# Optimization experiments

Measured on AMD Instinct MI355X. Metric: run time of the kernel, lower is better.

The kernel has to match this reference:

```python
import jax, jax.numpy as jnp
import numpy as np

B, A, HR = 2, 180, 512
H_OUT = W_OUT = 512


def setup_inputs() -> dict:
    key = jax.random.key(0)
    k1, = jax.random.split(key, 1)
    sino = jax.random.normal(k1, (B, A, HR), dtype=jnp.float32)
    angles_deg = jnp.linspace(0.0, 180.0, A, endpoint=False, dtype=jnp.float32)
    return {"sino": sino, "angles_deg": angles_deg, "H": H_OUT, "W": W_OUT}


def _forward(sino, angles_deg, H, W):
    Bn, An, Hr = sino.shape
    pad = int(1.0 * 0.1 * min(H, W))  # pad_ratio = 1.0
    Hp, Wp = H + 2 * pad, W + 2 * pad

    # --- F.interpolate bilinear, align_corners=False: (A,B,Hr,1) -> (A,B,Hp,Wp).
    # Input width is 1, so width interp replicates the single column; only height interp matters.
    src = jnp.clip((jnp.arange(Hp, dtype=jnp.float32) + 0.5) * (Hr / Hp) - 0.5, 0.0, Hr - 1)
    i0 = jnp.floor(src).astype(jnp.int32)
    i1 = jnp.minimum(i0 + 1, Hr - 1)
    wH = src - i0.astype(jnp.float32)
    p = jnp.transpose(sino, (1, 0, 2)).astype(jnp.float32)  # (A,B,Hr)
    col = p[:, :, i0] * (1.0 - wH) + p[:, :, i1] * wH       # (A,B,Hp)
    proj = jnp.broadcast_to(col[:, :, :, None], (An, Bn, Hp, Wp))  # (A,B,Hp,Wp)

    # --- affine_grid (align_corners=False), sign = -1
    th = -jnp.deg2rad(angles_deg)
    c, s = jnp.cos(th), jnp.sin(th)                          # (A,)
    xs = (jnp.arange(Wp, dtype=jnp.float32) + 0.5) * (2.0 / Wp) - 1.0
    ys = (jnp.arange(Hp, dtype=jnp.float32) + 0.5) * (2.0 / Hp) - 1.0
    gx = c[:, None, None] * xs[None, None, :] - s[:, None, None] * ys[None, :, None]  # (A,Hp,Wp)
    gy = s[:, None, None] * xs[None, None, :] + c[:, None, None] * ys[None, :, None]

    # --- grid_sample bilinear, zeros padding, align_corners=False
    ix = ((gx + 1.0) * Wp - 1.0) * 0.5
    iy = ((gy + 1.0) * Hp - 1.0) * 0.5
    x0 = jnp.floor(ix).astype(jnp.int32); x1 = x0 + 1
    y0 = jnp.floor(iy).astype(jnp.int32); y1 = y0 + 1
    wx = ix - x0.astype(jnp.float32)
    wy = iy - y0.astype(jnp.float32)

    def corner(img, xi, yi, w):  # img (B,Hp,Wp); idx/w (Hp,Wp)
        valid = (xi >= 0) & (xi <= Wp - 1) & (yi >= 0) & (yi <= Hp - 1)
        xc = jnp.clip(xi, 0, Wp - 1)
        yc = jnp.clip(yi, 0, Hp - 1)
        return img[:, yc, xc] * (w * valid.astype(jnp.float32))[None]

    def sample(img, x0a, x1a, y0a, y1a, wxa, wya):
        return (corner(img, x0a, y0a, (1 - wxa) * (1 - wya)) +
                corner(img, x1a, y0a, wxa * (1 - wya)) +
                corner(img, x0a, y1a, (1 - wxa) * wya) +
                corner(img, x1a, y1a, wxa * wya))

    xr = jax.vmap(sample)(proj, x0, x1, y0, y1, wx, wy)      # (A,B,Hp,Wp)
    acc = xr.sum(axis=0) / (An + 1e-06)                      # (B,Hp,Wp)
    acc = acc[:, None, :, :]                                 # (B,1,Hp,Wp)
    if pad > 0:
        acc = acc[:, :, pad:Hp - pad, pad:Wp - pad]
    return acc


def reference(sino, angles_deg, H, W):
    return _forward(sino, angles_deg, H, W)
```

## Files before the change

### kernel.cpp

```cpp
#include <hip/hip_runtime.h>
#include <hip/hip_fp16.h>
#include <math.h>

#define B_N   2
#define A_N   180
#define HR_N  512
#define H_OUT 512
#define W_OUT 512
#define PAD   51
#define HP    614
#define WP    614
#define GUARD 80
#define HPP   (HP + 2*GUARD)
#define NPIX  (H_OUT * W_OUT)

#define TILE  16
#define CH    30
#define NCH   (A_N / CH)
#define WIN   24


__device__ __forceinline__ float col_val(const float* __restrict__ sino,
                                         int b, int a, int yy) {
    if (yy < 0 || yy >= HP) return 0.0f;
    float src = ((float)yy + 0.5f) * ((float)HR_N / (float)HP) - 0.5f;
    src = fminf(fmaxf(src, 0.0f), (float)(HR_N - 1));
    int i0 = (int)floorf(src);
    int i1 = min(i0 + 1, HR_N - 1);
    float wH = src - (float)i0;
    const float* srow = sino + ((size_t)b * A_N + a) * HR_N;
    return srow[i0] * (1.0f - wH) + srow[i1] * wH;
}

__global__ void prep_kernel(const float* __restrict__ sino,
                            const float* __restrict__ angles,
                            uint2* __restrict__ pk2,
                            float2* __restrict__ tg) {
    int idx = blockIdx.x * blockDim.x + threadIdx.x;
    if (idx < A_N) {
        float th = -angles[idx] * (float)(M_PI / 180.0);
        tg[idx] = make_float2(cosf(th), sinf(th));
    }
    const int total = A_N * HPP;
    if (idx < total) {
        int y = idx % HPP;
        int a = idx / HPP;
        int yy = y - GUARD;
        float v00 = col_val(sino, 0, a, yy);
        float v10 = col_val(sino, 1, a, yy);
        float v01 = col_val(sino, 0, a, yy + 1);
        float v11 = col_val(sino, 1, a, yy + 1);
        __half2 lo = __floats2half2_rn(v00, v10);
        __half2 hi = __floats2half2_rn(v01, v11);
        uint2 u;
        u.x = *(unsigned int*)&lo;
        u.y = *(unsigned int*)&hi;
        pk2[idx] = u;
    }
}

template <bool INTERIOR>
__device__ __forceinline__ void bp_body(const uint2* __restrict__ pk2,
                                        const float2* __restrict__ tgv,
                                        uint2* __restrict__ s_win,
                                        const int* __restrict__ s_base,
                                        int t, float X, float Y, float Xc, float Yc,
                                        float& acc0, float& acc1) {
    for (int ch = 0; ch < NCH; ++ch) {
        int a0 = ch * CH;
        for (int e = t; e < CH * WIN; e += 256) {
            int la = e / WIN;
            int j  = e - la * WIN;
            int a  = a0 + la;
            s_win[e] = pk2[(size_t)a * HPP + (GUARD + s_base[a] + j)];
        }
        __syncthreads();

#pragma unroll 6
        for (int la = 0; la < CH; ++la) {
            float2 cs = tgv[a0 + la];
            float c = cs.x, s = cs.y;
            float iyc   = fmaf(s, Xc, fmaf(c, Yc, 306.5f));
            float basef = floorf(iyc);
            float iyp   = fmaf(s, X, fmaf(c, Y, 317.5f));
            float f  = iyp - basef;
            int   li = (int)f;
            float wy = f - (float)li;

            uint2 cv = s_win[la * WIN + li];
            __half2 lo = *(__half2*)&cv.x;
            __half2 hi = *(__half2*)&cv.y;
            float c00 = __low2float(lo), c10 = __high2float(lo);
            float c01 = __low2float(hi), c11 = __high2float(hi);

            if (INTERIOR) {
                acc0 = fmaf(wy, c01 - c00, acc0 + c00);
                acc1 = fmaf(wy, c11 - c10, acc1 + c10);
            } else {
                float ix = fmaf(c, X, fmaf(-s, Y, 306.5f));
                float xf = fminf(fmaxf(ix + 1.0f, 0.0f), 1.0f)
                         * fminf(fmaxf((float)WP - ix, 0.0f), 1.0f);
                float t0 = fmaf(wy, c01 - c00, c00);
                float t1 = fmaf(wy, c11 - c10, c10);
                acc0 = fmaf(xf, t0, acc0);
                acc1 = fmaf(xf, t1, acc1);
            }
        }
        __syncthreads();
    }
}

__global__ __launch_bounds__(256) void bp_kernel(const uint2* __restrict__ pk2,
                                                 const float2* __restrict__ tgv,
                                                 float* __restrict__ out) {
    __shared__ uint2 s_win[CH * WIN];
    __shared__ int   s_base[A_N];

    int t  = threadIdx.x;
    int tx = blockIdx.x, ty = blockIdx.y;
    float Xc = (float)(tx * TILE) - 248.0f;
    float Yc = (float)(ty * TILE) - 248.0f;

    if (t < A_N) {
        float2 cs = tgv[t];
        float iyc = fmaf(cs.y, Xc, fmaf(cs.x, Yc, 306.5f));
        s_base[t] = (int)floorf(iyc) - 11;
    }

    int lx = t & (TILE - 1);
    int ly = t >> 4;
    float X = (float)(tx * TILE + lx) - 255.5f;
    float Y = (float)(ty * TILE + ly) - 255.5f;

    float acc0 = 0.0f, acc1 = 0.0f;
    __syncthreads();

    bool interior = (Xc * Xc + Yc * Yc) <= 87500.0f;
    if (interior)
        bp_body<true >(pk2, tgv, s_win, s_base, t, X, Y, Xc, Yc, acc0, acc1);
    else
        bp_body<false>(pk2, tgv, s_win, s_base, t, X, Y, Xc, Yc, acc0, acc1);

    const float inv = 1.0f / (180.0f + 1e-6f);
    int idx = (ty * TILE + ly) * W_OUT + (tx * TILE + lx);
    out[idx]        = acc0 * inv;
    out[NPIX + idx] = acc1 * inv;
}

extern "C" void kernel_launch(void* const* d_in, const int* in_sizes, int n_in,
                              void* d_out, int out_size, void* d_ws, size_t ws_size,
                              hipStream_t stream) {
    const float* sino   = (const float*)d_in[0];
    const float* angles = (const float*)d_in[1];
    char*   ws  = (char*)d_ws;
    uint2*  pk2 = (uint2*)ws;
    float2* tg  = (float2*)(ws + (size_t)A_N * HPP * sizeof(uint2));

    const int total = A_N * HPP;
    prep_kernel<<<(total + 255) / 256, 256, 0, stream>>>(sino, angles, pk2, tg);

    dim3 grid(W_OUT / TILE, H_OUT / TILE);
    bp_kernel<<<grid, 256, 0, stream>>>(pk2, tg, (float*)d_out);
}
```

Measured before the change: 91.38 us.

## Split angle loop across two block halves with atomic accumulation

Each tile is now processed by two blocks, each handling half of the angles, and the partial sums are combined with atomicAdd into a zeroed output. This doubles the block count from 1024 to 2048 so more work is in flight per CU. It also precomputes per-angle cos, sin and window base in shared memory as a float4, removing per-iteration floor and recomputation. The cost is an extra memset, atomic writes, and duplicated per-block setup.

```diff
diff --git a/kernel.cpp b/kernel.cpp
--- a/kernel.cpp
+++ b/kernel.cpp
@@ -14,10 +14,11 @@
 #define HPP   (HP + 2*GUARD)
 #define NPIX  (H_OUT * W_OUT)
 
-#define TILE  16
-#define CH    30
-#define NCH   (A_N / CH)
-#define WIN   24
+#define TILE   16
+#define HALF_A 90
+#define CH     30
+#define NCHH   (HALF_A / CH)
+#define WIN    24
 
 
 __device__ __forceinline__ float col_val(const float* __restrict__ sino,
@@ -60,30 +61,28 @@
 }
 
 template <bool INTERIOR>
-__device__ __forceinline__ void bp_body(const uint2* __restrict__ pk2,
-                                        const float2* __restrict__ tgv,
+__device__ __forceinline__ void bp_body(const uint2* __restrict__ pkh,
+                                        const float4* __restrict__ s_ang,
+                                        const int* __restrict__ s_base,
                                         uint2* __restrict__ s_win,
-                                        const int* __restrict__ s_base,
-                                        int t, float X, float Y, float Xc, float Yc,
+                                        int t, float X, float Y,
                                         float& acc0, float& acc1) {
-    for (int ch = 0; ch < NCH; ++ch) {
+    for (int ch = 0; ch < NCHH; ++ch) {
         int a0 = ch * CH;
         for (int e = t; e < CH * WIN; e += 256) {
             int la = e / WIN;
             int j  = e - la * WIN;
             int a  = a0 + la;
-            s_win[e] = pk2[(size_t)a * HPP + (GUARD + s_base[a] + j)];
+            s_win[e] = pkh[(size_t)a * HPP + (GUARD + s_base[a] + j)];
         }
         __syncthreads();
 
 #pragma unroll 6
         for (int la = 0; la < CH; ++la) {
-            float2 cs = tgv[a0 + la];
-            float c = cs.x, s = cs.y;
-            float iyc   = fmaf(s, Xc, fmaf(c, Yc, 306.5f));
-            float basef = floorf(iyc);
-            float iyp   = fmaf(s, X, fmaf(c, Y, 317.5f));
-            float f  = iyp - basef;
+            float4 ang = s_ang[a0 + la];
+            float c = ang.x, s = ang.y, fb = ang.z;
+            float iy = fmaf(s, X, fmaf(c, Y, 306.5f));
+            float f  = iy - fb;
             int   li = (int)f;
             float wy = f - (float)li;
 
@@ -100,10 +99,8 @@
                 float ix = fmaf(c, X, fmaf(-s, Y, 306.5f));
                 float xf = fminf(fmaxf(ix + 1.0f, 0.0f), 1.0f)
                          * fminf(fmaxf((float)WP - ix, 0.0f), 1.0f);
-                float t0 = fmaf(wy, c01 - c00, c00);
-                float t1 = fmaf(wy, c11 - c10, c10);
-                acc0 = fmaf(xf, t0, acc0);
-                acc1 = fmaf(xf, t1, acc1);
+                acc0 = fmaf(xf, fmaf(wy, c01 - c00, c00), acc0);
+                acc1 = fmaf(xf, fmaf(wy, c11 - c10, c10), acc1);
             }
         }
         __syncthreads();
@@ -113,18 +110,22 @@
 __global__ __launch_bounds__(256) void bp_kernel(const uint2* __restrict__ pk2,
                                                  const float2* __restrict__ tgv,
                                                  float* __restrict__ out) {
-    __shared__ uint2 s_win[CH * WIN];
-    __shared__ int   s_base[A_N];
+    __shared__ float4 s_ang[HALF_A];
+    __shared__ int    s_base[HALF_A];
+    __shared__ uint2  s_win[CH * WIN];
 
-    int t  = threadIdx.x;
-    int tx = blockIdx.x, ty = blockIdx.y;
+    int t    = threadIdx.x;
+    int tx   = blockIdx.x & 31, ty = blockIdx.x >> 5;
+    int half = blockIdx.y;
     float Xc = (float)(tx * TILE) - 248.0f;
     float Yc = (float)(ty * TILE) - 248.0f;
 
-    if (t < A_N) {
-        float2 cs = tgv[t];
+    if (t < HALF_A) {
+        float2 cs = tgv[half * HALF_A + t];
         float iyc = fmaf(cs.y, Xc, fmaf(cs.x, Yc, 306.5f));
-        s_base[t] = (int)floorf(iyc) - 11;
+        int base = (int)floorf(iyc) - 11;
+        s_ang[t]  = make_float4(cs.x, cs.y, (float)base, 0.0f);
+        s_base[t] = base;
     }
 
     int lx = t & (TILE - 1);
@@ -135,16 +136,18 @@
     float acc0 = 0.0f, acc1 = 0.0f;
     __syncthreads();
 
+    const uint2* pkh = pk2 + (size_t)(half * HALF_A) * HPP;
+
     bool interior = (Xc * Xc + Yc * Yc) <= 87500.0f;
     if (interior)
-        bp_body<true >(pk2, tgv, s_win, s_base, t, X, Y, Xc, Yc, acc0, acc1);
+        bp_body<true >(pkh, s_ang, s_base, s_win, t, X, Y, acc0, acc1);
     else
-        bp_body<false>(pk2, tgv, s_win, s_base, t, X, Y, Xc, Yc, acc0, acc1);
+        bp_body<false>(pkh, s_ang, s_base, s_win, t, X, Y, acc0, acc1);
 
     const float inv = 1.0f / (180.0f + 1e-6f);
     int idx = (ty * TILE + ly) * W_OUT + (tx * TILE + lx);
-    out[idx]        = acc0 * inv;
-    out[NPIX + idx] = acc1 * inv;
+    atomicAdd(&out[idx],        acc0 * inv);
+    atomicAdd(&out[NPIX + idx], acc1 * inv);
 }
 
 extern "C" void kernel_launch(void* const* d_in, const int* in_sizes, int n_in,
@@ -159,6 +162,8 @@
     const int total = A_N * HPP;
     prep_kernel<<<(total + 255) / 256, 256, 0, stream>>>(sino, angles, pk2, tg);
 
-    dim3 grid(W_OUT / TILE, H_OUT / TILE);
+    hipMemsetAsync(d_out, 0, (size_t)out_size * sizeof(float), stream);
+
+    dim3 grid(1024, 2);
     bp_kernel<<<grid, 256, 0, stream>>>(pk2, tg, (float*)d_out);
 }
```

Measured after the change: 86.00 us. -5.9%, faster.

## Split angles across two half-blocks with smaller tiles and packed-half interpolation

Applied to the files above, without the earlier changes.

The backprojection block now covers a 16x8 pixel tile. Its two 128-thread halves each process half of the angles, and the partial sums are combined through shared memory at the end. Per-angle constants (cos, sin, offset relative to the window base) are precomputed into shared memory, which shortens the inner-loop address math. The window shrinks to 20 entries and the vertical interpolation runs with packed half2 FMA. This adds more blocks for better occupancy, and the half-precision interpolation weight risks a small accuracy loss.

```diff
diff --git a/kernel.cpp b/kernel.cpp
--- a/kernel.cpp
+++ b/kernel.cpp
@@ -14,10 +14,12 @@
 #define HPP   (HP + 2*GUARD)
 #define NPIX  (H_OUT * W_OUT)
 
-#define TILE  16
-#define CH    30
-#define NCH   (A_N / CH)
-#define WIN   24
+#define TW     16
+#define TH     8
+#define HALF_A 90
+#define CH     30
+#define NCH    (HALF_A / CH)
+#define WIN    20
 
 
 __device__ __forceinline__ float col_val(const float* __restrict__ sino,
@@ -59,92 +61,103 @@
     }
 }
 
-template <bool INTERIOR>
-__device__ __forceinline__ void bp_body(const uint2* __restrict__ pk2,
-                                        const float2* __restrict__ tgv,
-                                        uint2* __restrict__ s_win,
-                                        const int* __restrict__ s_base,
-                                        int t, float X, float Y, float Xc, float Yc,
-                                        float& acc0, float& acc1) {
-    for (int ch = 0; ch < NCH; ++ch) {
-        int a0 = ch * CH;
-        for (int e = t; e < CH * WIN; e += 256) {
-            int la = e / WIN;
-            int j  = e - la * WIN;
-            int a  = a0 + la;
-            s_win[e] = pk2[(size_t)a * HPP + (GUARD + s_base[a] + j)];
-        }
-        __syncthreads();
-
-#pragma unroll 6
-        for (int la = 0; la < CH; ++la) {
-            float2 cs = tgv[a0 + la];
-            float c = cs.x, s = cs.y;
-            float iyc   = fmaf(s, Xc, fmaf(c, Yc, 306.5f));
-            float basef = floorf(iyc);
-            float iyp   = fmaf(s, X, fmaf(c, Y, 317.5f));
-            float f  = iyp - basef;
-            int   li = (int)f;
-            float wy = f - (float)li;
-
-            uint2 cv = s_win[la * WIN + li];
-            __half2 lo = *(__half2*)&cv.x;
-            __half2 hi = *(__half2*)&cv.y;
-            float c00 = __low2float(lo), c10 = __high2float(lo);
-            float c01 = __low2float(hi), c11 = __high2float(hi);
-
-            if (INTERIOR) {
-                acc0 = fmaf(wy, c01 - c00, acc0 + c00);
-                acc1 = fmaf(wy, c11 - c10, acc1 + c10);
-            } else {
-                float ix = fmaf(c, X, fmaf(-s, Y, 306.5f));
-                float xf = fminf(fmaxf(ix + 1.0f, 0.0f), 1.0f)
-                         * fminf(fmaxf((float)WP - ix, 0.0f), 1.0f);
-                float t0 = fmaf(wy, c01 - c00, c00);
-                float t1 = fmaf(wy, c11 - c10, c10);
-                acc0 = fmaf(xf, t0, acc0);
-                acc1 = fmaf(xf, t1, acc1);
-            }
-        }
-        __syncthreads();
-    }
-}
-
-__global__ __launch_bounds__(256) void bp_kernel(const uint2* __restrict__ pk2,
-                                                 const float2* __restrict__ tgv,
-                                                 float* __restrict__ out) {
-    __shared__ uint2 s_win[CH * WIN];
-    __shared__ int   s_base[A_N];
+__global__ __launch_bounds__(256, 8) void bp_kernel(const uint2* __restrict__ pk2,
+                                                    const float2* __restrict__ tgv,
+                                                    float* __restrict__ out) {
+    __shared__ float4 s_ang[A_N];
+    __shared__ int    s_base[A_N];
+    __shared__ uint2  s_win[2 * CH * WIN];
+    __shared__ float  s_red[2][128];
 
     int t  = threadIdx.x;
     int tx = blockIdx.x, ty = blockIdx.y;
-    float Xc = (float)(tx * TILE) - 248.0f;
-    float Yc = (float)(ty * TILE) - 248.0f;
+    float Xc = (float)(tx * TW) - 248.0f;
+    float Yc = (float)(ty * TH) - 252.0f;
 
     if (t < A_N) {
         float2 cs = tgv[t];
         float iyc = fmaf(cs.y, Xc, fmaf(cs.x, Yc, 306.5f));
-        s_base[t] = (int)floorf(iyc) - 11;
+        int base = (int)floorf(iyc) - 9;
+        s_ang[t]  = make_float4(cs.x, cs.y, 306.5f - (float)base, 0.0f);
+        s_base[t] = base;
     }
 
-    int lx = t & (TILE - 1);
-    int ly = t >> 4;
-    float X = (float)(tx * TILE + lx) - 255.5f;
-    float Y = (float)(ty * TILE + ly) - 255.5f;
+    int half = t >> 7;
+    int tt   = t & 127;
+    int lx = tt & (TW - 1), ly = tt >> 4;
+    float X = (float)(tx * TW + lx) - 255.5f;
+    float Y = (float)(ty * TH + ly) - 255.5f;
 
     float acc0 = 0.0f, acc1 = 0.0f;
     __syncthreads();
 
     bool interior = (Xc * Xc + Yc * Yc) <= 87500.0f;
-    if (interior)
-        bp_body<true >(pk2, tgv, s_win, s_base, t, X, Y, Xc, Yc, acc0, acc1);
-    else
-        bp_body<false>(pk2, tgv, s_win, s_base, t, X, Y, Xc, Yc, acc0, acc1);
 
-    const float inv = 1.0f / (180.0f + 1e-6f);
-    int idx = (ty * TILE + ly) * W_OUT + (tx * TILE + lx);
-    out[idx]        = acc0 * inv;
-    out[NPIX + idx] = acc1 * inv;
+    for (int ch = 0; ch < NCH; ++ch) {
+        for (int e = t; e < 2 * CH * WIN; e += 256) {
+            int hh = e / (CH * WIN);
+            int r  = e - hh * (CH * WIN);
+            int la = r / WIN;
+            int j  = r - la * WIN;
+            int a  = hh * HALF_A + ch * CH + la;
+            s_win[e] = pk2[(size_t)a * HPP + (GUARD + s_base[a] + j)];
+        }
+        __syncthreads();
+
+        const int aoff = half * HALF_A + ch * CH;
+        const int woff = half * (CH * WIN);
+        if (interior) {
+#pragma unroll 5
+            for (int la = 0; la < CH; ++la) {
+                float4 ang = s_ang[aoff + la];
+                float f  = fmaf(ang.y, X, fmaf(ang.x, Y, ang.z));
+                int   li = (int)f;
+                float wy = f - (float)li;
+                uint2 cv = s_win[woff + la * WIN + li];
+                __half2 lo = *(__half2*)&cv.x;
+                __half2 hi = *(__half2*)&cv.y;
+                __half2 d  = __hsub2(hi, lo);
+                __half2 wv = __float2half2_rn(wy);
+                __half2 r2 = __hfma2(wv, d, lo);
+                acc0 += __low2float(r2);
+                acc1 += __high2float(r2);
+            }
+        } else {
+#pragma unroll 5
+            for (int la = 0; la < CH; ++la) {
+                float4 ang = s_ang[aoff + la];
+                float f  = fmaf(ang.y, X, fmaf(ang.x, Y, ang.z));
+                int   li = (int)f;
+                float wy = f - (float)li;
+                uint2 cv = s_win[woff + la * WIN + li];
+                __half2 lo = *(__half2*)&cv.x;
+                __half2 hi = *(__half2*)&cv.y;
+                __half2 d  = __hsub2(hi, lo);
+                __half2 wv = __float2half2_rn(wy);
+                __half2 r2 = __hfma2(wv, d, lo);
+                float ix = fmaf(ang.x, X, fmaf(-ang.y, Y, 306.5f));
+                float xf = fminf(fmaxf(ix + 1.0f, 0.0f), 1.0f)
+                         * fminf(fmaxf((float)WP - ix, 0.0f), 1.0f);
+                acc0 = fmaf(xf, __low2float(r2), acc0);
+                acc1 = fmaf(xf, __high2float(r2), acc1);
+            }
+        }
+        __syncthreads();
+    }
+
+    if (half) {
+        s_red[0][tt] = acc0;
+        s_red[1][tt] = acc1;
+    }
+    __syncthreads();
+    if (!half) {
+        const float inv = 1.0f / (180.0f + 1e-6f);
+        float a0 = (acc0 + s_red[0][tt]) * inv;
+        float a1 = (acc1 + s_red[1][tt]) * inv;
+        int idx = (ty * TH + ly) * W_OUT + (tx * TW + lx);
+        out[idx]        = a0;
+        out[NPIX + idx] = a1;
+    }
 }
 
 extern "C" void kernel_launch(void* const* d_in, const int* in_sizes, int n_in,
@@ -159,6 +172,6 @@
     const int total = A_N * HPP;
     prep_kernel<<<(total + 255) / 256, 256, 0, stream>>>(sino, angles, pk2, tg);
 
-    dim3 grid(W_OUT / TILE, H_OUT / TILE);
+    dim3 grid(W_OUT / TW, H_OUT / TH);
     bp_kernel<<<grid, 256, 0, stream>>>(pk2, tg, (float*)d_out);
 }
```

After: 84.67 us. 1.08x faster.

## Split angles across wavefronts, 4 pixels per thread, half2 interp, shared reduction

Applied to the files above, without the earlier changes.

The backprojection kernel now loads all 180 angle windows into shared memory in a single pass, removing the per-chunk reload and barrier loop. Each of the four wavefronts handles a quarter of the angles, and each thread covers four adjacent x pixels, stepping the coordinate incrementally by sin/cos. Bilinear interpolation is done with packed half2 FMA. The partial sums from the four wavefronts are combined through shared memory, and the result is written with float4 stores. This cuts synchronisation and per-pixel address work, but it uses more shared memory and adds a reduction step. Interpolating in fp16 also lowers accuracy.

```diff
diff --git a/kernel.cpp b/kernel.cpp
--- a/kernel.cpp
+++ b/kernel.cpp
@@ -15,8 +15,7 @@
 #define NPIX  (H_OUT * W_OUT)
 
 #define TILE  16
-#define CH    30
-#define NCH   (A_N / CH)
+#define QA    45
 #define WIN   24
 
 
@@ -59,62 +58,12 @@
     }
 }
 
-template <bool INTERIOR>
-__device__ __forceinline__ void bp_body(const uint2* __restrict__ pk2,
-                                        const float2* __restrict__ tgv,
-                                        uint2* __restrict__ s_win,
-                                        const int* __restrict__ s_base,
-                                        int t, float X, float Y, float Xc, float Yc,
-                                        float& acc0, float& acc1) {
-    for (int ch = 0; ch < NCH; ++ch) {
-        int a0 = ch * CH;
-        for (int e = t; e < CH * WIN; e += 256) {
-            int la = e / WIN;
-            int j  = e - la * WIN;
-            int a  = a0 + la;
-            s_win[e] = pk2[(size_t)a * HPP + (GUARD + s_base[a] + j)];
-        }
-        __syncthreads();
-
-#pragma unroll 6
-        for (int la = 0; la < CH; ++la) {
-            float2 cs = tgv[a0 + la];
-            float c = cs.x, s = cs.y;
-            float iyc   = fmaf(s, Xc, fmaf(c, Yc, 306.5f));
-            float basef = floorf(iyc);
-            float iyp   = fmaf(s, X, fmaf(c, Y, 317.5f));
-            float f  = iyp - basef;
-            int   li = (int)f;
-            float wy = f - (float)li;
-
-            uint2 cv = s_win[la * WIN + li];
-            __half2 lo = *(__half2*)&cv.x;
-            __half2 hi = *(__half2*)&cv.y;
-            float c00 = __low2float(lo), c10 = __high2float(lo);
-            float c01 = __low2float(hi), c11 = __high2float(hi);
-
-            if (INTERIOR) {
-                acc0 = fmaf(wy, c01 - c00, acc0 + c00);
-                acc1 = fmaf(wy, c11 - c10, acc1 + c10);
-            } else {
-                float ix = fmaf(c, X, fmaf(-s, Y, 306.5f));
-                float xf = fminf(fmaxf(ix + 1.0f, 0.0f), 1.0f)
-                         * fminf(fmaxf((float)WP - ix, 0.0f), 1.0f);
-                float t0 = fmaf(wy, c01 - c00, c00);
-                float t1 = fmaf(wy, c11 - c10, c10);
-                acc0 = fmaf(xf, t0, acc0);
-                acc1 = fmaf(xf, t1, acc1);
-            }
-        }
-        __syncthreads();
-    }
-}
-
-__global__ __launch_bounds__(256) void bp_kernel(const uint2* __restrict__ pk2,
-                                                 const float2* __restrict__ tgv,
-                                                 float* __restrict__ out) {
-    __shared__ uint2 s_win[CH * WIN];
-    __shared__ int   s_base[A_N];
+__global__ __launch_bounds__(256, 4) void bp_kernel(const uint2* __restrict__ pk2,
+                                                    const float2* __restrict__ tgv,
+                                                    float* __restrict__ out) {
+    __shared__ float2 s_tg[A_N];
+    __shared__ int    s_base[A_N];
+    __shared__ uint2  s_win[A_N * WIN];
 
     int t  = threadIdx.x;
     int tx = blockIdx.x, ty = blockIdx.y;
@@ -123,28 +72,108 @@
 
     if (t < A_N) {
         float2 cs = tgv[t];
+        s_tg[t] = cs;
         float iyc = fmaf(cs.y, Xc, fmaf(cs.x, Yc, 306.5f));
         s_base[t] = (int)floorf(iyc) - 11;
     }
-
-    int lx = t & (TILE - 1);
-    int ly = t >> 4;
-    float X = (float)(tx * TILE + lx) - 255.5f;
-    float Y = (float)(ty * TILE + ly) - 255.5f;
-
-    float acc0 = 0.0f, acc1 = 0.0f;
     __syncthreads();
 
+    for (int e = t; e < A_N * WIN; e += 256) {
+        int wid = e / WIN;
+        int j   = e - wid * WIN;
+        s_win[e] = pk2[(size_t)wid * HPP + (GUARD + s_base[wid] + j)];
+    }
+    __syncthreads();
+
+    int q    = t >> 6;
+    int lane = t & 63;
+    int xq   = lane & 3;
+    int yy   = lane >> 2;
+    int x0   = tx * TILE + xq * 4;
+    int y0   = ty * TILE + yy;
+    float X  = (float)x0 - 255.5f;
+    float Y  = (float)y0 - 255.5f;
+
+    float2 acc[4] = {{0,0},{0,0},{0,0},{0,0}};
+
     bool interior = (Xc * Xc + Yc * Yc) <= 87500.0f;
-    if (interior)
-        bp_body<true >(pk2, tgv, s_win, s_base, t, X, Y, Xc, Yc, acc0, acc1);
-    else
-        bp_body<false>(pk2, tgv, s_win, s_base, t, X, Y, Xc, Yc, acc0, acc1);
+    const int abase = q * QA;
+    const uint2* winq = s_win + abase * WIN;
 
-    const float inv = 1.0f / (180.0f + 1e-6f);
-    int idx = (ty * TILE + ly) * W_OUT + (tx * TILE + lx);
-    out[idx]        = acc0 * inv;
-    out[NPIX + idx] = acc1 * inv;
+    if (interior) {
+#pragma unroll 5
+        for (int la = 0; la < QA; ++la) {
+            float2 cs = s_tg[abase + la];
+            float c = cs.x, s = cs.y;
+            float iyc = fmaf(s, Xc, fmaf(c, Yc, 306.5f));
+            float Kf  = 317.5f - floorf(iyc);
+            float f0  = fmaf(s, X, fmaf(c, Y, Kf));
+            float f1 = f0 + s, f2 = f1 + s, f3 = f2 + s;
+            float fg[4] = {f0, f1, f2, f3};
+#pragma unroll
+            for (int g = 0; g < 4; ++g) {
+                int   li = (int)fg[g];
+                float wy = fg[g] - (float)li;
+                uint2 cv = winq[la * WIN + li];
+                __half2 lo = *(__half2*)&cv.x;
+                __half2 hi = *(__half2*)&cv.y;
+                __half2 r2 = __hfma2(__float2half2_rn(wy), __hsub2(hi, lo), lo);
+                acc[g].x += __low2float(r2);
+                acc[g].y += __high2float(r2);
+            }
+        }
+    } else {
+#pragma unroll 5
+        for (int la = 0; la < QA; ++la) {
+            float2 cs = s_tg[abase + la];
+            float c = cs.x, s = cs.y;
+            float iyc = fmaf(s, Xc, fmaf(c, Yc, 306.5f));
+            float Kf  = 317.5f - floorf(iyc);
+            float f0  = fmaf(s, X, fmaf(c, Y, Kf));
+            float ix0 = fmaf(c, X, fmaf(-s, Y, 306.5f));
+            float fg = f0, ixg = ix0;
+#pragma unroll
+            for (int g = 0; g < 4; ++g) {
+                int   li = (int)fg;
+                float wy = fg - (float)li;
+                uint2 cv = winq[la * WIN + li];
+                __half2 lo = *(__half2*)&cv.x;
+                __half2 hi = *(__half2*)&cv.y;
+                __half2 r2 = __hfma2(__float2half2_rn(wy), __hsub2(hi, lo), lo);
+                float xf = fminf(fmaxf(ixg + 1.0f, 0.0f), 1.0f)
+                         * fminf(fmaxf((float)WP - ixg, 0.0f), 1.0f);
+                acc[g].x = fmaf(xf, __low2float(r2),  acc[g].x);
+                acc[g].y = fmaf(xf, __high2float(r2), acc[g].y);
+                fg += s; ixg += c;
+            }
+        }
+    }
+
+    __syncthreads();
+    float* red = (float*)s_win;
+    int px = yy * TILE + xq * 4;
+    if (q != 0) {
+        int o = (q - 1) * 512;
+#pragma unroll
+        for (int g = 0; g < 4; ++g) {
+            red[o + px + g]       = acc[g].x;
+            red[o + 256 + px + g] = acc[g].y;
+        }
+    }
+    __syncthreads();
+    if (q == 0) {
+        const float inv = 1.0f / (180.0f + 1e-6f);
+        float4 r0, r1;
+        float* p0 = &r0.x; float* p1 = &r1.x;
+#pragma unroll
+        for (int g = 0; g < 4; ++g) {
+            p0[g] = (acc[g].x + red[px + g]       + red[512 + px + g]       + red[1024 + px + g])       * inv;
+            p1[g] = (acc[g].y + red[256 + px + g] + red[512 + 256 + px + g] + red[1024 + 256 + px + g]) * inv;
+        }
+        int idx = y0 * W_OUT + x0;
+        *(float4*)&out[idx]        = r0;
+        *(float4*)&out[NPIX + idx] = r1;
+    }
 }
 
 extern "C" void kernel_launch(void* const* d_in, const int* in_sizes, int n_in,
```

Measured after the change: 84.91 us. 7.1% less time.
